# Kernel optimization log

Hardware: AMD Instinct MI355X
Metric: run time of the kernel (lower is better)

## Reference

```python
import jax, jax.numpy as jnp
import numpy as np

ALPHA = 10.0
DELTA = 0.0005
N = 16777216  # array_length


def setup_inputs() -> dict:
    key = jax.random.key(0)
    k1, k2 = jax.random.split(key)
    # learned parameter: in the original module this is initialized to linspace(0,1,N);
    # we use uniform [0,1] so the piecewise-linear search path is non-degenerate.
    indices = jax.random.uniform(k1, (N,), dtype=jnp.float32)
    array = jax.random.normal(k2, (N,), dtype=jnp.float32)
    return {"indices": indices, "array": array}


def reference(indices, array):
    # clamp learned knot positions to [0, 1]
    clamped = jnp.clip(indices, 0.0, 1.0)
    # piecewise-linear function f with x-knots = clamped, y-values = array.
    # jnp.interp requires ascending knots, so sort (x, y) pairs by x.
    order = jnp.argsort(clamped)
    xs = clamped[order]
    ys = array[order]
    # vectorized version of the per-index loop:
    #   left_item = f(clamped[i-1] + delta), this_item = f(clamped[i] - delta)
    q_left = clamped[:-1] + DELTA   # [N-1]
    q_this = clamped[1:] - DELTA    # [N-1]
    f_left = jnp.interp(q_left, xs, ys)
    f_this = jnp.interp(q_this, xs, ys)
    gap = jnp.maximum(f_left - f_this, 0.0)
    return ALPHA * jnp.sum(gap)
```

## Files before the change

### kernel.cpp

```cpp
#include <hip/hip_runtime.h>
#include <stdint.h>

#define ALPHA_C 10.0f
#define DELTA_C 0.0005f

typedef unsigned long long u64;
typedef unsigned u32;
typedef unsigned short u16;

#define KB2   (1u << 22)
#define NREG  8192
#define FPR   512
#define CAP   4096
#define Q38MAX ((1ULL << 38) - 1)

#define OLDKB (1u << 22)
#define SCAN_BLOCKS 1024
#define SCAN_TPB 256
#define SCAN_PER_THREAD 16

__device__ __forceinline__ float clamp01(float x) {
    return fminf(fmaxf(x, 0.0f), 1.0f);
}
__device__ __forceinline__ u64 q38_of(float x) {
    double d = (double)clamp01(x) * 274877906944.0;
    u64 q = (u64)d;
    return q > Q38MAX ? Q38MAX : q;
}
__device__ __forceinline__ u16 f2bf(float f) {
    u32 b = __float_as_uint(f);
    return (u16)((b + 0x8000u) >> 16);
}
__device__ __forceinline__ float bf2f(u32 h) {
    return __uint_as_float(h << 16);
}


__global__ void __launch_bounds__(256) k_hist(const float* __restrict__ ind,
                                              u32* __restrict__ cnt8k, int n) {
    __shared__ u32 lh[NREG];
    for (int k = threadIdx.x; k < (int)NREG; k += 256) lh[k] = 0;
    __syncthreads();
    int stride = gridDim.x * blockDim.x;
    for (int i = blockIdx.x * blockDim.x + threadIdx.x; i < n; i += stride)
        atomicAdd(&lh[(u32)(q38_of(ind[i]) >> 25)], 1u);
    __syncthreads();
    for (int k = threadIdx.x; k < (int)NREG; k += 256) {
        u32 v = lh[k];
        if (v) atomicAdd(&cnt8k[k], v);
    }
}

__global__ void __launch_bounds__(1024) k_scan8k(u32* __restrict__ cnt8k) {
    __shared__ u32 lds[1024];
    int tid = threadIdx.x;
    int base = tid * 8;
    u32 v[8]; u32 tot = 0;
#pragma unroll
    for (int k = 0; k < 8; ++k) { v[k] = cnt8k[base + k]; tot += v[k]; }
    lds[tid] = tot;
    __syncthreads();
    u32 x = tot;
    for (int s = 1; s < 1024; s <<= 1) {
        u32 y = (tid >= s) ? lds[tid - s] : 0u;
        __syncthreads();
        x += y; lds[tid] = x;
        __syncthreads();
    }
    u32 run = x - tot;
#pragma unroll
    for (int k = 0; k < 8; ++k) { u32 c = v[k]; cnt8k[base + k] = run; run += c; }
}

__global__ void k_coarse(const float* __restrict__ ind, const float* __restrict__ arr,
                         u32* __restrict__ cnt8k,
                         u32* __restrict__ recx, u64* __restrict__ reciy, int n) {
    int i = blockIdx.x * blockDim.x + threadIdx.x;
    if (i < n) {
        float x = ind[i];
        u32 r = (u32)(q38_of(x) >> 25);
        u32 e = atomicAdd(&cnt8k[r], 1u);
        recx[e] = __float_as_uint(x);
        reciy[e] = ((u64)(u32)i << 16) | (u64)f2bf(arr[i]);
    }
}

__global__ void __launch_bounds__(512) k_fine(const u32* __restrict__ cnt8k,
                                              u16* __restrict__ foff16,
                                              const u32* __restrict__ recx,
                                              u64* __restrict__ reciy_fdata) {
    __shared__ u32 sx[CAP];
    __shared__ u64 siy[CAP];
    __shared__ u32 incl[FPR];
    __shared__ u32 lexcl[FPR];
    __shared__ u32 lcnt[FPR];
    int r = blockIdx.x;
    u32 s = (r == 0) ? 0u : cnt8k[r - 1];
    u32 e = cnt8k[r];
    u32 cnt = e - s; if (cnt > CAP) cnt = CAP;
    for (u32 j = threadIdx.x; j < cnt; j += 512) { sx[j] = recx[s + j]; siy[j] = reciy_fdata[s + j]; }
    incl[threadIdx.x] = 0;
    lcnt[threadIdx.x] = 0;
    __syncthreads();
    for (u32 j = threadIdx.x; j < cnt; j += 512) {
        u32 lb = (u32)((q38_of(__uint_as_float(sx[j])) >> 16) & (FPR - 1));
        atomicAdd(&incl[lb], 1u);
    }
    __syncthreads();
    u32 myc = incl[threadIdx.x];
    u32 x = myc;
    for (int st = 1; st < FPR; st <<= 1) {
        u32 y = (threadIdx.x >= (u32)st) ? incl[threadIdx.x - st] : 0u;
        __syncthreads();
        x += y; incl[threadIdx.x] = x;
        __syncthreads();
    }
    lexcl[threadIdx.x] = x - myc;
    foff16[r * FPR + threadIdx.x] = (u16)x;
    __syncthreads();
    for (u32 j = threadIdx.x; j < cnt; j += 512) {
        u64 q = q38_of(__uint_as_float(sx[j]));
        u32 lb = (u32)((q >> 16) & (FPR - 1));
        u32 p = s + lexcl[lb] + atomicAdd(&lcnt[lb], 1u);
        u64 iy = siy[j];
        reciy_fdata[p] = ((q & 0xFFFFULL) << 40) | ((iy & 0xFFFFULL) << 24) | (iy >> 16);
    }
}

__device__ __forceinline__ void bucket_range(u32 b, const u32* __restrict__ cnt8k,
                                             const u16* __restrict__ foff16,
                                             u32* s, u32* e) {
    u32 r = b >> 9;
    u32 rbase = r ? cnt8k[r - 1] : 0u;
    u32 lb = b & (FPR - 1);
    *s = rbase + (lb ? (u32)foff16[b - 1] : 0u);
    *e = rbase + (u32)foff16[b];
}

__device__ float feval_q(u64 qq, const u32* __restrict__ cnt8k,
                         const u16* __restrict__ foff16, const u64* __restrict__ fdata) {
    u32 qb = (u32)(qq >> 16);
    u32 ql = (u32)(qq & 0xFFFFu);
    u32 s, e;
    bucket_range(qb, cnt8k, foff16, &s, &e);
    long long loK = -1;
    u64 hiK = ~0ULL;
    float loY = 0.0f, hiY = 0.0f;
    for (u32 p = s; p < e; ++p) {
        u64 d = fdata[p];
        u32 xlo = (u32)(d >> 40);
        u64 key = ((((u64)qb << 16) | xlo) << 24) | (d & 0xFFFFFFULL);
        float y = bf2f((u32)(d >> 24) & 0xFFFFu);
        if (xlo <= ql) { if ((long long)key >= loK) { loK = (long long)key; loY = y; } }
        else           { if (key < hiK)             { hiK = key;            hiY = y; } }
    }
    if (loK < 0) {
        u32 bl = qb;
        while (bl > 0) {
            --bl;
            u32 s2, e2;
            bucket_range(bl, cnt8k, foff16, &s2, &e2);
            if (e2 > s2) {
                for (u32 p = s2; p < e2; ++p) {
                    u64 d = fdata[p];
                    u64 key = ((((u64)bl << 16) | (d >> 40)) << 24) | (d & 0xFFFFFFULL);
                    if ((long long)key >= loK) { loK = (long long)key; loY = bf2f((u32)(d >> 24) & 0xFFFFu); }
                }
                break;
            }
        }
    }
    if (hiK == ~0ULL) {
        u32 br = qb;
        while (br < KB2 - 1) {
            ++br;
            u32 s2, e2;
            bucket_range(br, cnt8k, foff16, &s2, &e2);
            if (e2 > s2) {
                for (u32 p = s2; p < e2; ++p) {
                    u64 d = fdata[p];
                    u64 key = ((((u64)br << 16) | (d >> 40)) << 24) | (d & 0xFFFFFFULL);
                    if (key < hiK) { hiK = key; hiY = bf2f((u32)(d >> 24) & 0xFFFFu); }
                }
                break;
            }
        }
    }
    if (loK < 0) return hiY;
    if (hiK == ~0ULL) return loY;
    u64 loQ = (u64)loK >> 24;
    u64 hiQ = hiK >> 24;
    if (hiQ == loQ) return loY;
    float dq = (float)(qq - loQ);
    float dd = (float)(hiQ - loQ);
    return loY + (dq / dd) * (hiY - loY);
}

__global__ void __launch_bounds__(512) k_eval(const u32* __restrict__ cnt8k,
        const u16* __restrict__ foff16, const u64* __restrict__ fdata,
        u32* __restrict__ oval) {
    __shared__ u32 fend[FPR];
    int r = blockIdx.x;
    u32 s = r ? cnt8k[r - 1] : 0u;
    u32 e = cnt8k[r];
    fend[threadIdx.x] = s + (u32)foff16[r * FPR + threadIdx.x];
    __syncthreads();
    for (u32 t = s + threadIdx.x; t < e; t += 512) {
        u64 d = fdata[t];
        u32 lo = 0;
#pragma unroll
        for (u32 st = 256; st; st >>= 1) if (t >= fend[lo + st - 1]) lo += st;
        u64 xq = (((u64)((u32)r * FPR + lo)) << 16) | (d >> 40);
        u32 i = (u32)(d & 0xFFFFFFu);
        float x = (float)((double)xq * 3.63797880709171295e-12);
        float qpf = x + DELTA_C;
        float qmf = x - DELTA_C;
        u64 qp = q38_of(qpf);
        u64 qm = q38_of(qmf);
        float fp = feval_q(qp, cnt8k, foff16, fdata);
        float fm = feval_q(qm, cnt8k, foff16, fdata);
        oval[i] = ((u32)f2bf(fp) << 16) | (u32)f2bf(fm);
    }
}

__global__ void __launch_bounds__(256) k_pair2(const u32* __restrict__ oval,
                                               float* __restrict__ out, int n) {
    int stride = gridDim.x * blockDim.x;
    float sum = 0.0f;
    for (int j = blockIdx.x * blockDim.x + threadIdx.x; j < n - 1; j += stride) {
        u32 a = oval[j], b = oval[j + 1];
        sum += fmaxf(bf2f(a >> 16) - bf2f(b & 0xFFFFu), 0.0f);
    }
    float w = sum;
    for (int s = 32; s > 0; s >>= 1) w += __shfl_down(w, s, 64);
    __shared__ float wsum[4];
    if ((threadIdx.x & 63) == 0) wsum[threadIdx.x >> 6] = w;
    __syncthreads();
    if (threadIdx.x == 0)
        atomicAdd(out, ALPHA_C * (wsum[0] + wsum[1] + wsum[2] + wsum[3]));
}


__device__ __forceinline__ int bucket_of(float x) {
    int b = (int)(x * (float)OLDKB);
    b = b < 0 ? 0 : b;
    b = b > (int)OLDKB - 1 ? (int)OLDKB - 1 : b;
    return b;
}

__global__ void scan1(u32* __restrict__ off, u32* __restrict__ bsums) {
    __shared__ u32 lds[SCAN_TPB];
    int base = blockIdx.x * (SCAN_TPB * SCAN_PER_THREAD) + threadIdx.x * SCAN_PER_THREAD;
    u32 v[SCAN_PER_THREAD];
    u32 tot = 0;
#pragma unroll
    for (int k = 0; k < SCAN_PER_THREAD; ++k) { v[k] = off[base + k]; tot += v[k]; }
    lds[threadIdx.x] = tot;
    __syncthreads();
    u32 x = tot;
    for (int s = 1; s < SCAN_TPB; s <<= 1) {
        u32 y = (threadIdx.x >= (u32)s) ? lds[threadIdx.x - s] : 0u;
        __syncthreads();
        x += y; lds[threadIdx.x] = x;
        __syncthreads();
    }
    if (threadIdx.x == SCAN_TPB - 1) bsums[blockIdx.x] = x;
    u32 run = x - tot;
#pragma unroll
    for (int k = 0; k < SCAN_PER_THREAD; ++k) { u32 c = v[k]; off[base + k] = run; run += c; }
}

__global__ void scan2(u32* __restrict__ bsums) {
    __shared__ u32 lds[SCAN_BLOCKS];
    int tid = threadIdx.x;
    u32 v = bsums[tid];
    lds[tid] = v;
    __syncthreads();
    u32 x = v;
    for (int s = 1; s < SCAN_BLOCKS; s <<= 1) {
        u32 y = (tid >= s) ? lds[tid - s] : 0u;
        __syncthreads();
        x += y; lds[tid] = x;
        __syncthreads();
    }
    bsums[tid] = x - v;
}

__global__ void scan3(u32* __restrict__ off, const u32* __restrict__ bsums) {
    int base = blockIdx.x * (SCAN_TPB * SCAN_PER_THREAD);
    u32 add = bsums[blockIdx.x];
#pragma unroll
    for (int k = 0; k < SCAN_PER_THREAD; ++k)
        off[base + k * SCAN_TPB + threadIdx.x] += add;
}

__global__ void hist_kernel(const float* __restrict__ ind, u32* __restrict__ off, int n) {
    int i = blockIdx.x * blockDim.x + threadIdx.x;
    if (i < n) atomicAdd(&off[bucket_of(clamp01(ind[i]))], 1u);
}

__global__ void scatter_kernel(const float* __restrict__ ind, const float* __restrict__ arr,
                               u32* __restrict__ off, float2* __restrict__ buck, int n) {
    int i = blockIdx.x * blockDim.x + threadIdx.x;
    if (i < n) {
        float x = clamp01(ind[i]);
        u32 p = atomicAdd(&off[bucket_of(x)], 1u);
        buck[p] = make_float2(x, arr[i]);
    }
}

__device__ float feval(float q, const u32* __restrict__ off, const float2* __restrict__ buck) {
    int b = bucket_of(q);
    u32 s = (b == 0) ? 0u : off[b - 1];
    u32 e = off[b];
    float loX = -1e30f, loY = 0.0f, hiX = 1e30f, hiY = 0.0f;
    for (u32 u = s; u < e; ++u) {
        float2 p = buck[u];
        if (p.x <= q) { if (p.x >= loX) { loX = p.x; loY = p.y; } }
        else          { if (p.x <  hiX) { hiX = p.x; hiY = p.y; } }
    }
    if (loX == -1e30f) {
        int bl = b;
        while (bl > 0) {
            --bl;
            u32 s2 = (bl == 0) ? 0u : off[bl - 1];
            u32 e2 = off[bl];
            if (e2 > s2) {
                for (u32 u = s2; u < e2; ++u) {
                    float2 p = buck[u];
                    if (p.x >= loX) { loX = p.x; loY = p.y; }
                }
                break;
            }
        }
    }
    if (hiX == 1e30f) {
        int br = b;
        while (br < (int)OLDKB - 1) {
            ++br;
            u32 s2 = off[br - 1];
            u32 e2 = off[br];
            if (e2 > s2) {
                for (u32 u = s2; u < e2; ++u) {
                    float2 p = buck[u];
                    if (p.x < hiX) { hiX = p.x; hiY = p.y; }
                }
                break;
            }
        }
    }
    if (loX == -1e30f) return hiY;
    if (hiX ==  1e30f) return loY;
    return loY + (q - loX) * (hiY - loY) / (hiX - loX);
}

__global__ void query_kernel(const float* __restrict__ ind, const u32* __restrict__ off,
                             const float2* __restrict__ buck, float* __restrict__ out, int nterm) {
    int j = blockIdx.x * blockDim.x + threadIdx.x;
    float term = 0.0f;
    if (j < nterm) {
        float c0 = clamp01(ind[j]);
        float c1 = clamp01(ind[j + 1]);
        float fa = feval(c0 + DELTA_C, off, buck);
        float fb = feval(c1 - DELTA_C, off, buck);
        term = fmaxf(fa - fb, 0.0f);
    }
    float w = term;
    for (int s = 32; s > 0; s >>= 1) w += __shfl_down(w, s, 64);
    __shared__ float wsum[4];
    if ((threadIdx.x & 63) == 0) wsum[threadIdx.x >> 6] = w;
    __syncthreads();
    if (threadIdx.x == 0) atomicAdd(out, ALPHA_C * (wsum[0] + wsum[1] + wsum[2] + wsum[3]));
}


extern "C" void kernel_launch(void* const* d_in, const int* in_sizes, int n_in,
                              void* d_out, int out_size, void* d_ws, size_t ws_size,
                              hipStream_t stream) {
    const float* ind = (const float*)d_in[0];
    const float* arr = (const float*)d_in[1];
    float* out = (float*)d_out;
    int n = in_sizes[0];

    const int tpb = 256;
    int nblk = (n + tpb - 1) / tpb;
    uint8_t* w = (uint8_t*)d_ws;

    const size_t FOFF_SZ = (size_t)KB2 * 2;
    const size_t AUX = (size_t)1 << 20;
    size_t SZ8 = (size_t)n * 8, SZ4 = (size_t)n * 4;
    size_t base = FOFF_SZ + AUX;
    size_t need = base + SZ8 + SZ4;

    if (n <= (1 << 24) && ws_size >= need) {
        u16* foff16 = (u16*)w;
        u32* cnt8k  = (u32*)(w + FOFF_SZ);
        u64* reciy  = (u64*)(w + base);
        u32* recx   = (u32*)(w + base + SZ8);
        u32* oval   = (u32*)recx;

        hipMemsetAsync(cnt8k, 0, NREG * 4, stream);
        hipMemsetAsync(out, 0, sizeof(float) * (size_t)out_size, stream);

        k_hist<<<512, 256, 0, stream>>>(ind, cnt8k, n);
        k_scan8k<<<1, 1024, 0, stream>>>(cnt8k);
        k_coarse<<<nblk, tpb, 0, stream>>>(ind, arr, cnt8k, recx, reciy, n);
        k_fine<<<NREG, 512, 0, stream>>>(cnt8k, foff16, recx, reciy);
        k_eval<<<NREG, 512, 0, stream>>>(cnt8k, foff16, reciy, oval);
        k_pair2<<<2048, 256, 0, stream>>>(oval, out, n);
    } else {
        const size_t FO = (size_t)OLDKB * 4;
        u32* off = (u32*)w;
        u32* bsums = (u32*)(w + FO);
        float2* buck = (float2*)(w + FO + 4096);

        hipMemsetAsync(off, 0, FO, stream);
        hipMemsetAsync(out, 0, sizeof(float) * (size_t)out_size, stream);

        hist_kernel<<<nblk, tpb, 0, stream>>>(ind, off, n);
        scan1<<<SCAN_BLOCKS, SCAN_TPB, 0, stream>>>(off, bsums);
        scan2<<<1, SCAN_BLOCKS, 0, stream>>>(bsums);
        scan3<<<SCAN_BLOCKS, SCAN_TPB, 0, stream>>>(off, bsums);
        scatter_kernel<<<nblk, tpb, 0, stream>>>(ind, arr, off, buck, n);
        int nterm = n - 1;
        query_kernel<<<(nterm + tpb - 1) / tpb, tpb, 0, stream>>>(ind, off, buck, out, nterm);
    }
}
```

Measured before the change: 1.611 ms.

## Pack sort records into single u64 keys with 16k regions and partitioned scatter

Doubles the coarse regions to 16384 of 256 fine buckets each. Each record becomes one 64-bit word holding the low 24 bits of the quantized x, the index and the bf16 y, so the separate x array goes away. Fine sorting and neighbour lookup now compare packed words directly, and the eval kernel no longer needs a binary search to recover the fine bucket. The coarse scatter splits its grid into 8 key-range partitions, each reading all inputs, to improve write locality in exchange for extra input re-reads.

New measurement: 1.774 ms. 10.1% more time.

```diff
diff --git a/kernel.cpp b/kernel.cpp
--- a/kernel.cpp
+++ b/kernel.cpp
@@ -8,10 +8,11 @@
 typedef unsigned u32;
 typedef unsigned short u16;
 
+#define NREG2 16384
 #define KB2   (1u << 22)
-#define NREG  8192
-#define FPR   512
-#define CAP   4096
+#define FPR2  256
+#define CAP2  2048
+#define NPART 8
 #define Q38MAX ((1ULL << 38) - 1)
 
 #define OLDKB (1u << 22)
@@ -37,27 +38,27 @@
 
 
 __global__ void __launch_bounds__(256) k_hist(const float* __restrict__ ind,
-                                              u32* __restrict__ cnt8k, int n) {
-    __shared__ u32 lh[NREG];
-    for (int k = threadIdx.x; k < (int)NREG; k += 256) lh[k] = 0;
+                                              u32* __restrict__ cnt16k, int n) {
+    __shared__ u32 lh[NREG2];
+    for (int k = threadIdx.x; k < (int)NREG2; k += 256) lh[k] = 0;
     __syncthreads();
     int stride = gridDim.x * blockDim.x;
     for (int i = blockIdx.x * blockDim.x + threadIdx.x; i < n; i += stride)
-        atomicAdd(&lh[(u32)(q38_of(ind[i]) >> 25)], 1u);
-    __syncthreads();
-    for (int k = threadIdx.x; k < (int)NREG; k += 256) {
+        atomicAdd(&lh[(u32)(q38_of(ind[i]) >> 24)], 1u);
+    __syncthreads();
+    for (int k = threadIdx.x; k < (int)NREG2; k += 256) {
         u32 v = lh[k];
-        if (v) atomicAdd(&cnt8k[k], v);
-    }
-}
-
-__global__ void __launch_bounds__(1024) k_scan8k(u32* __restrict__ cnt8k) {
+        if (v) atomicAdd(&cnt16k[k], v);
+    }
+}
+
+__global__ void __launch_bounds__(1024) k_scan16k(u32* __restrict__ c) {
     __shared__ u32 lds[1024];
     int tid = threadIdx.x;
-    int base = tid * 8;
-    u32 v[8]; u32 tot = 0;
+    int base = tid * 16;
+    u32 v[16]; u32 tot = 0;
 #pragma unroll
-    for (int k = 0; k < 8; ++k) { v[k] = cnt8k[base + k]; tot += v[k]; }
+    for (int k = 0; k < 16; ++k) { v[k] = c[base + k]; tot += v[k]; }
     lds[tid] = tot;
     __syncthreads();
     u32 x = tot;
@@ -69,156 +70,140 @@
     }
     u32 run = x - tot;
 #pragma unroll
-    for (int k = 0; k < 8; ++k) { u32 c = v[k]; cnt8k[base + k] = run; run += c; }
-}
-
-__global__ void k_coarse(const float* __restrict__ ind, const float* __restrict__ arr,
-                         u32* __restrict__ cnt8k,
-                         u32* __restrict__ recx, u64* __restrict__ reciy, int n) {
-    int i = blockIdx.x * blockDim.x + threadIdx.x;
-    if (i < n) {
+    for (int k = 0; k < 16; ++k) { u32 cc = v[k]; c[base + k] = run; run += cc; }
+}
+
+__global__ void __launch_bounds__(256) k_coarse(const float* __restrict__ ind,
+                                                const float* __restrict__ arr,
+                                                u32* __restrict__ cnt16k,
+                                                u64* __restrict__ rec, int n) {
+    u32 p = blockIdx.x & (NPART - 1);
+    u32 g = blockIdx.x >> 3;
+    u32 nb = gridDim.x >> 3;
+    int stride = nb * 256;
+    for (int i = g * 256 + threadIdx.x; i < n; i += stride) {
         float x = ind[i];
-        u32 r = (u32)(q38_of(x) >> 25);
-        u32 e = atomicAdd(&cnt8k[r], 1u);
-        recx[e] = __float_as_uint(x);
-        reciy[e] = ((u64)(u32)i << 16) | (u64)f2bf(arr[i]);
-    }
-}
-
-__global__ void __launch_bounds__(512) k_fine(const u32* __restrict__ cnt8k,
+        u64 q = q38_of(x);
+        u32 r = (u32)(q >> 24);
+        if ((r >> 11) == p) {
+            u32 e = atomicAdd(&cnt16k[r], 1u);
+            rec[e] = ((q & 0xFFFFFFULL) << 40) | ((u64)(u32)i << 16) | (u64)f2bf(arr[i]);
+        }
+    }
+}
+
+__global__ void __launch_bounds__(256) k_fine(const u32* __restrict__ cnt16k,
                                               u16* __restrict__ foff16,
-                                              const u32* __restrict__ recx,
-                                              u64* __restrict__ reciy_fdata) {
-    __shared__ u32 sx[CAP];
-    __shared__ u64 siy[CAP];
-    __shared__ u32 incl[FPR];
-    __shared__ u32 lexcl[FPR];
-    __shared__ u32 lcnt[FPR];
+                                              u64* __restrict__ rec) {
+    __shared__ u64 srec[CAP2];
+    __shared__ u32 incl[FPR2];
+    __shared__ u32 lexcl[FPR2];
+    __shared__ u32 lcnt[FPR2];
     int r = blockIdx.x;
-    u32 s = (r == 0) ? 0u : cnt8k[r - 1];
-    u32 e = cnt8k[r];
-    u32 cnt = e - s; if (cnt > CAP) cnt = CAP;
-    for (u32 j = threadIdx.x; j < cnt; j += 512) { sx[j] = recx[s + j]; siy[j] = reciy_fdata[s + j]; }
+    u32 s = r ? cnt16k[r - 1] : 0u;
+    u32 e = cnt16k[r];
+    u32 cnt = e - s; if (cnt > CAP2) cnt = CAP2;
+    for (u32 j = threadIdx.x; j < cnt; j += 256) srec[j] = rec[s + j];
     incl[threadIdx.x] = 0;
     lcnt[threadIdx.x] = 0;
     __syncthreads();
-    for (u32 j = threadIdx.x; j < cnt; j += 512) {
-        u32 lb = (u32)((q38_of(__uint_as_float(sx[j])) >> 16) & (FPR - 1));
-        atomicAdd(&incl[lb], 1u);
-    }
+    for (u32 j = threadIdx.x; j < cnt; j += 256)
+        atomicAdd(&incl[(u32)(srec[j] >> 56)], 1u);
     __syncthreads();
     u32 myc = incl[threadIdx.x];
     u32 x = myc;
-    for (int st = 1; st < FPR; st <<= 1) {
+    for (int st = 1; st < FPR2; st <<= 1) {
         u32 y = (threadIdx.x >= (u32)st) ? incl[threadIdx.x - st] : 0u;
         __syncthreads();
         x += y; incl[threadIdx.x] = x;
         __syncthreads();
     }
     lexcl[threadIdx.x] = x - myc;
-    foff16[r * FPR + threadIdx.x] = (u16)x;
-    __syncthreads();
-    for (u32 j = threadIdx.x; j < cnt; j += 512) {
-        u64 q = q38_of(__uint_as_float(sx[j]));
-        u32 lb = (u32)((q >> 16) & (FPR - 1));
-        u32 p = s + lexcl[lb] + atomicAdd(&lcnt[lb], 1u);
-        u64 iy = siy[j];
-        reciy_fdata[p] = ((q & 0xFFFFULL) << 40) | ((iy & 0xFFFFULL) << 24) | (iy >> 16);
-    }
-}
-
-__device__ __forceinline__ void bucket_range(u32 b, const u32* __restrict__ cnt8k,
+    foff16[r * FPR2 + threadIdx.x] = (u16)x;
+    __syncthreads();
+    for (u32 j = threadIdx.x; j < cnt; j += 256) {
+        u64 d = srec[j];
+        u32 lb = (u32)(d >> 56);
+        u32 pp = s + lexcl[lb] + atomicAdd(&lcnt[lb], 1u);
+        rec[pp] = d;
+    }
+}
+
+__device__ __forceinline__ void bucket_range(u32 b, const u32* __restrict__ cnt16k,
                                              const u16* __restrict__ foff16,
                                              u32* s, u32* e) {
-    u32 r = b >> 9;
-    u32 rbase = r ? cnt8k[r - 1] : 0u;
-    u32 lb = b & (FPR - 1);
+    u32 r = b >> 8;
+    u32 rbase = r ? cnt16k[r - 1] : 0u;
+    u32 lb = b & (FPR2 - 1);
     *s = rbase + (lb ? (u32)foff16[b - 1] : 0u);
     *e = rbase + (u32)foff16[b];
 }
 
-__device__ float feval_q(u64 qq, const u32* __restrict__ cnt8k,
-                         const u16* __restrict__ foff16, const u64* __restrict__ fdata) {
+__device__ float feval_q(u64 qq, const u32* __restrict__ cnt16k,
+                         const u16* __restrict__ foff16, const u64* __restrict__ rec) {
     u32 qb = (u32)(qq >> 16);
-    u32 ql = (u32)(qq & 0xFFFFu);
+    u64 Tm = ((qq & 0xFFFFFFULL) << 40) | 0xFFFFFFFFFFULL;
     u32 s, e;
-    bucket_range(qb, cnt8k, foff16, &s, &e);
-    long long loK = -1;
-    u64 hiK = ~0ULL;
-    float loY = 0.0f, hiY = 0.0f;
+    bucket_range(qb, cnt16k, foff16, &s, &e);
+    u64 lo = 0, hi = ~0ULL;
+    u32 loB = qb, hiB = qb;
     for (u32 p = s; p < e; ++p) {
-        u64 d = fdata[p];
-        u32 xlo = (u32)(d >> 40);
-        u64 key = ((((u64)qb << 16) | xlo) << 24) | (d & 0xFFFFFFULL);
-        float y = bf2f((u32)(d >> 24) & 0xFFFFu);
-        if (xlo <= ql) { if ((long long)key >= loK) { loK = (long long)key; loY = y; } }
-        else           { if (key < hiK)             { hiK = key;            hiY = y; } }
-    }
-    if (loK < 0) {
+        u64 d = rec[p];
+        if (d <= Tm) { if (d > lo) lo = d; }
+        else         { if (d < hi) hi = d; }
+    }
+    if (lo == 0) {
         u32 bl = qb;
         while (bl > 0) {
             --bl;
             u32 s2, e2;
-            bucket_range(bl, cnt8k, foff16, &s2, &e2);
+            bucket_range(bl, cnt16k, foff16, &s2, &e2);
             if (e2 > s2) {
-                for (u32 p = s2; p < e2; ++p) {
-                    u64 d = fdata[p];
-                    u64 key = ((((u64)bl << 16) | (d >> 40)) << 24) | (d & 0xFFFFFFULL);
-                    if ((long long)key >= loK) { loK = (long long)key; loY = bf2f((u32)(d >> 24) & 0xFFFFu); }
-                }
+                for (u32 p = s2; p < e2; ++p) { u64 d = rec[p]; if (d > lo) lo = d; }
+                loB = bl;
                 break;
             }
         }
     }
-    if (hiK == ~0ULL) {
+    if (hi == ~0ULL) {
         u32 br = qb;
         while (br < KB2 - 1) {
             ++br;
             u32 s2, e2;
-            bucket_range(br, cnt8k, foff16, &s2, &e2);
+            bucket_range(br, cnt16k, foff16, &s2, &e2);
             if (e2 > s2) {
-                for (u32 p = s2; p < e2; ++p) {
-                    u64 d = fdata[p];
-                    u64 key = ((((u64)br << 16) | (d >> 40)) << 24) | (d & 0xFFFFFFULL);
-                    if (key < hiK) { hiK = key; hiY = bf2f((u32)(d >> 24) & 0xFFFFu); }
-                }
+                for (u32 p = s2; p < e2; ++p) { u64 d = rec[p]; if (d < hi) hi = d; }
+                hiB = br;
                 break;
             }
         }
     }
-    if (loK < 0) return hiY;
-    if (hiK == ~0ULL) return loY;
-    u64 loQ = (u64)loK >> 24;
-    u64 hiQ = hiK >> 24;
-    if (hiQ == loQ) return loY;
+    float loY = bf2f((u32)(lo & 0xFFFFu));
+    float hiY = bf2f((u32)(hi & 0xFFFFu));
+    if (lo == 0)     return hiY;
+    if (hi == ~0ULL) return loY;
+    u64 loQ = ((u64)(loB >> 8) << 24) | (lo >> 40);
+    u64 hiQ = ((u64)(hiB >> 8) << 24) | (hi >> 40);
     float dq = (float)(qq - loQ);
     float dd = (float)(hiQ - loQ);
     return loY + (dq / dd) * (hiY - loY);
 }
 
-__global__ void __launch_bounds__(512) k_eval(const u32* __restrict__ cnt8k,
-        const u16* __restrict__ foff16, const u64* __restrict__ fdata,
+__global__ void __launch_bounds__(256) k_eval(const u32* __restrict__ cnt16k,
+        const u16* __restrict__ foff16, const u64* __restrict__ rec,
         u32* __restrict__ oval) {
-    __shared__ u32 fend[FPR];
     int r = blockIdx.x;
-    u32 s = r ? cnt8k[r - 1] : 0u;
-    u32 e = cnt8k[r];
-    fend[threadIdx.x] = s + (u32)foff16[r * FPR + threadIdx.x];
-    __syncthreads();
-    for (u32 t = s + threadIdx.x; t < e; t += 512) {
-        u64 d = fdata[t];
-        u32 lo = 0;
-#pragma unroll
-        for (u32 st = 256; st; st >>= 1) if (t >= fend[lo + st - 1]) lo += st;
-        u64 xq = (((u64)((u32)r * FPR + lo)) << 16) | (d >> 40);
-        u32 i = (u32)(d & 0xFFFFFFu);
-        float x = (float)((double)xq * 3.63797880709171295e-12);
+    u32 s = r ? cnt16k[r - 1] : 0u;
+    u32 e = cnt16k[r];
+    for (u32 t = s + threadIdx.x; t < e; t += 256) {
+        u64 d = rec[t];
+        u64 xq = ((u64)(u32)r << 24) | (d >> 40);
+        u32 i = (u32)(d >> 16) & 0xFFFFFFu;
+        float x = (float)((double)xq * (1.0 / 274877906944.0));
         float qpf = x + DELTA_C;
         float qmf = x - DELTA_C;
-        u64 qp = q38_of(qpf);
-        u64 qm = q38_of(qmf);
-        float fp = feval_q(qp, cnt8k, foff16, fdata);
-        float fm = feval_q(qm, cnt8k, foff16, fdata);
+        float fp = feval_q(q38_of(qpf), cnt16k, foff16, rec);
+        float fm = feval_q(q38_of(qmf), cnt16k, foff16, rec);
         oval[i] = ((u32)f2bf(fp) << 16) | (u32)f2bf(fm);
     }
 }
@@ -394,19 +379,18 @@
 
     if (n <= (1 << 24) && ws_size >= need) {
         u16* foff16 = (u16*)w;
-        u32* cnt8k  = (u32*)(w + FOFF_SZ);
-        u64* reciy  = (u64*)(w + base);
-        u32* recx   = (u32*)(w + base + SZ8);
-        u32* oval   = (u32*)recx;
-
-        hipMemsetAsync(cnt8k, 0, NREG * 4, stream);
+        u32* cnt16k = (u32*)(w + FOFF_SZ);
+        u64* rec    = (u64*)(w + base);
+        u32* oval   = (u32*)(w + base + SZ8);
+
+        hipMemsetAsync(cnt16k, 0, NREG2 * 4, stream);
         hipMemsetAsync(out, 0, sizeof(float) * (size_t)out_size, stream);
 
-        k_hist<<<512, 256, 0, stream>>>(ind, cnt8k, n);
-        k_scan8k<<<1, 1024, 0, stream>>>(cnt8k);
-        k_coarse<<<nblk, tpb, 0, stream>>>(ind, arr, cnt8k, recx, reciy, n);
-        k_fine<<<NREG, 512, 0, stream>>>(cnt8k, foff16, recx, reciy);
-        k_eval<<<NREG, 512, 0, stream>>>(cnt8k, foff16, reciy, oval);
+        k_hist<<<512, 256, 0, stream>>>(ind, cnt16k, n);
+        k_scan16k<<<1, 1024, 0, stream>>>(cnt16k);
+        k_coarse<<<2048, 256, 0, stream>>>(ind, arr, cnt16k, rec, n);
+        k_fine<<<NREG2, 256, 0, stream>>>(cnt16k, foff16, rec);
+        k_eval<<<NREG2, 256, 0, stream>>>(cnt16k, foff16, rec, oval);
         k_pair2<<<2048, 256, 0, stream>>>(oval, out, n);
     } else {
         const size_t FO = (size_t)OLDKB * 4;
```
